# Optimization experiments

Hardware: AMD Instinct MI355X
Metric: run time of the kernel (lower is better)

The kernel has to match this reference:

```python
import jax, jax.numpy as jnp
import numpy as np

SPATIAL_SHAPES = np.array([[128, 128], [64, 64], [32, 32], [16, 16]], dtype=np.int32)  # (H, W) per level
D_MODEL = 256
D_FFN = 1024
N_LEVELS = 4
N_HEADS = 8
N_POINTS = 4
HEAD_DIM = D_MODEL // N_HEADS
B = 2
LEN = int((SPATIAL_SHAPES[:, 0] * SPATIAL_SHAPES[:, 1]).sum())  # 21760


def layer_norm(x, g, b, eps=1e-5):
    mu = x.mean(-1, keepdims=True)
    var = ((x - mu) ** 2).mean(-1, keepdims=True)
    return (x - mu) / jnp.sqrt(var + eps) * g + b


def ms_deform_attn_core(value, sampling_locations, attention_weights):
    # value: [B, Len, M, D]; locations: [B, Lq, M, L, P, 2] in [0,1]; weights: [B, Lq, M, L, P]
    B_, _, M, D = value.shape
    Lq = sampling_locations.shape[1]
    P = sampling_locations.shape[4]
    out = jnp.zeros((B_, M, Lq, D), value.dtype)
    start = 0
    for lvl, (H, W) in enumerate(SPATIAL_SHAPES.tolist()):
        v = value[:, start:start + H * W].transpose(0, 2, 1, 3)  # [B, M, H*W, D]
        start += H * W
        loc = sampling_locations[:, :, :, lvl].transpose(0, 2, 1, 3, 4)  # [B, M, Lq, P, 2]
        # grid_sample semantics: align_corners=False, padding_mode='zeros'
        x = loc[..., 0] * W - 0.5
        y = loc[..., 1] * H - 0.5
        x0 = jnp.floor(x)
        y0 = jnp.floor(y)
        wx = (x - x0)[..., None]
        wy = (y - y0)[..., None]

        def gather(xi, yi):
            valid = ((xi >= 0) & (xi < W) & (yi >= 0) & (yi < H)).astype(value.dtype)
            idx = (jnp.clip(yi, 0, H - 1) * W + jnp.clip(xi, 0, W - 1)).astype(jnp.int32)
            idx = idx.reshape(B_, M, Lq * P)
            g = jnp.take_along_axis(v, idx[..., None], axis=2).reshape(B_, M, Lq, P, D)
            return g * valid[..., None]

        v00 = gather(x0, y0)
        v01 = gather(x0 + 1, y0)
        v10 = gather(x0, y0 + 1)
        v11 = gather(x0 + 1, y0 + 1)
        samp = (v00 * (1 - wx) + v01 * wx) * (1 - wy) + (v10 * (1 - wx) + v11 * wx) * wy
        w_l = attention_weights[:, :, :, lvl].transpose(0, 2, 1, 3)  # [B, M, Lq, P]
        out = out + (samp * w_l[..., None]).sum(axis=3)
    return out.transpose(0, 2, 1, 3).reshape(B_, Lq, M * D)


def setup_inputs() -> dict:
    key = jax.random.key(0)
    ks = jax.random.split(key, 16)
    f32 = jnp.float32

    def lin(k, fan_in, fan_out, scale=None):
        s = scale if scale is not None else 1.0 / np.sqrt(fan_in)
        return jax.random.normal(k, (fan_in, fan_out), f32) * s

    starts = np.concatenate([[0], np.cumsum(SPATIAL_SHAPES[:, 0] * SPATIAL_SHAPES[:, 1])[:-1]]).astype(np.int32)
    inp = {
        "src": jax.random.normal(ks[0], (B, LEN, D_MODEL), f32),
        "pos": jax.random.normal(ks[1], (B, LEN, D_MODEL), f32),
        "reference_points": jax.random.uniform(ks[2], (B, LEN, N_LEVELS, 2), f32),
        "spatial_shapes": jnp.asarray(SPATIAL_SHAPES),
        "level_start_index": jnp.asarray(starts),
        "norm1_g": jnp.ones((D_MODEL,), f32), "norm1_b": jnp.zeros((D_MODEL,), f32),
        "norm2_g": jnp.ones((D_MODEL,), f32), "norm2_b": jnp.zeros((D_MODEL,), f32),
        "W_value": lin(ks[3], D_MODEL, D_MODEL), "b_value": jnp.zeros((D_MODEL,), f32),
        "W_off": lin(ks[4], D_MODEL, N_HEADS * N_LEVELS * N_POINTS * 2, scale=0.01),
        "b_off": jax.random.normal(ks[5], (N_HEADS * N_LEVELS * N_POINTS * 2,), f32) * 0.01,
        "W_attn": lin(ks[6], D_MODEL, N_HEADS * N_LEVELS * N_POINTS),
        "b_attn": jnp.zeros((N_HEADS * N_LEVELS * N_POINTS,), f32),
        "W_out": lin(ks[7], D_MODEL, D_MODEL), "b_out": jnp.zeros((D_MODEL,), f32),
        "W_ffn1": lin(ks[8], D_MODEL, D_FFN), "b_ffn1": jnp.zeros((D_FFN,), f32),
        "W_ffn2": lin(ks[9], D_FFN, D_MODEL), "b_ffn2": jnp.zeros((D_MODEL,), f32),
    }
    return inp


def reference(src, pos, reference_points, spatial_shapes, level_start_index,
              norm1_g, norm1_b, norm2_g, norm2_b,
              W_value, b_value, W_off, b_off, W_attn, b_attn, W_out, b_out,
              W_ffn1, b_ffn1, W_ffn2, b_ffn2):
    B_, Lq, C = src.shape
    # pre-norm deformable self-attention; NOTE: value path uses un-normed src (faithful to source)
    q = layer_norm(src, norm1_g, norm1_b) + pos
    value = (src @ W_value + b_value).reshape(B_, Lq, N_HEADS, HEAD_DIM)
    offsets = (q @ W_off + b_off).reshape(B_, Lq, N_HEADS, N_LEVELS, N_POINTS, 2)
    attn = jax.nn.softmax((q @ W_attn + b_attn).reshape(B_, Lq, N_HEADS, N_LEVELS * N_POINTS), axis=-1)
    attn = attn.reshape(B_, Lq, N_HEADS, N_LEVELS, N_POINTS)
    offset_normalizer = spatial_shapes[..., ::-1].astype(src.dtype)  # (W, H) per level
    loc = reference_points[:, :, None, :, None, :] + offsets / offset_normalizer[None, None, None, :, None, :]
    attn_out = ms_deform_attn_core(value, loc, attn) @ W_out + b_out
    src = src + attn_out
    h = layer_norm(src, norm2_g, norm2_b)
    h = jax.nn.gelu(h @ W_ffn1 + b_ffn1, approximate=False) @ W_ffn2 + b_ffn2
    return src + h
```

## Files before the change

kernel.cpp:

```cpp
#include <hip/hip_runtime.h>
#include <hip/hip_bf16.h>
#include <math.h>

#define LEN_TOT 21760
#define BATCH 2
#define MROWS (BATCH * LEN_TOT)
#define DMODEL 256
#define DFFN 1024

typedef unsigned short ushort_t;
typedef __attribute__((ext_vector_type(8))) short short8;
typedef __attribute__((ext_vector_type(4))) short short4v;
typedef __attribute__((ext_vector_type(4))) float floatx4;
typedef __attribute__((address_space(3))) ushort_t lds_us;
typedef __attribute__((address_space(1))) const ushort_t glb_us;

__device__ __forceinline__ ushort_t f2b(float f) {
    unsigned u = __float_as_uint(f);
    unsigned r = (u + 0x7FFFu + ((u >> 16) & 1u)) >> 16;
    return (ushort_t)r;
}
__device__ __forceinline__ float b2f(ushort_t u) {
    return __uint_as_float(((unsigned)u) << 16);
}

__device__ __forceinline__ float gelu_f(float x) {
    float x3 = x * x * x;
    float t = fmaf(x3, 0.035677408136f, x * 0.7978845608028654f);
    float e = __expf(2.0f * t);
    float th = 1.0f - 2.0f / (e + 1.0f);
    return 0.5f * x * (1.0f + th);
}

__device__ __forceinline__ int xcd_swizzle(int b, int n) {
    int q8 = n >> 3, r8 = n & 7;
    int xcd = b & 7, idx = b >> 3;
    return (xcd < r8 ? xcd * (q8 + 1) : r8 * (q8 + 1) + (xcd - r8) * q8) + idx;
}

template<int CTRL>
__device__ __forceinline__ float dpp_f(float x) {
    return __int_as_float(__builtin_amdgcn_update_dpp(
        0, __float_as_int(x), CTRL, 0xF, 0xF, true));
}
__device__ __forceinline__ float swz16_f(float x) {
    return __int_as_float(__builtin_amdgcn_ds_swizzle(__float_as_int(x), 0x401F));
}

struct TP {
    const float* s[6];
    ushort_t*    d[6];
    int K[6];
    int N[6];
    int start[7];
};

__global__ __launch_bounds__(256) void transpose_convert(TP tp) {
    __shared__ float tile[32][33];
    int blk = blockIdx.x;
    int seg = 0;
    while (seg < 5 && blk >= tp.start[seg + 1]) seg++;
    int local = blk - tp.start[seg];
    int K = tp.K[seg], N = tp.N[seg];
    int tn = N >> 5;
    int k0 = (local / tn) << 5, n0 = (local % tn) << 5;
    int r = threadIdx.x >> 5, c = threadIdx.x & 31;
    const float* src = tp.s[seg];
    #pragma unroll
    for (int rr = r; rr < 32; rr += 8)
        tile[rr][c] = src[(size_t)(k0 + rr) * N + n0 + c];
    __syncthreads();
    ushort_t* dst = tp.d[seg];
    #pragma unroll
    for (int rr = r; rr < 32; rr += 8)
        dst[(size_t)(n0 + rr) * K + k0 + c] = f2b(tile[c][rr]);
}

__global__ __launch_bounds__(256) void ln_dual_kernel(
    const float* __restrict__ x, const float* __restrict__ g,
    const float* __restrict__ bb, const float* __restrict__ addv,
    ushort_t* __restrict__ y_bf, ushort_t* __restrict__ x_bf)
{
    int row  = blockIdx.x * 4 + (threadIdx.x >> 6);
    int lane = threadIdx.x & 63;
    size_t base = (size_t)row * DMODEL + lane * 4;
    float4 v = *(const float4*)(x + base);

    float s = v.x + v.y + v.z + v.w;
    #pragma unroll
    for (int o = 32; o; o >>= 1) s += __shfl_xor(s, o, 64);
    float mu = s * (1.0f / 256.0f);

    float d0 = v.x - mu, d1 = v.y - mu, d2 = v.z - mu, d3 = v.w - mu;
    float vs = d0*d0 + d1*d1 + d2*d2 + d3*d3;
    #pragma unroll
    for (int o = 32; o; o >>= 1) vs += __shfl_xor(vs, o, 64);
    float rstd = rsqrtf(vs * (1.0f / 256.0f) + 1e-5f);

    float4 gv = *(const float4*)(g  + lane * 4);
    float4 bv = *(const float4*)(bb + lane * 4);
    float o0 = d0 * rstd * gv.x + bv.x;
    float o1 = d1 * rstd * gv.y + bv.y;
    float o2 = d2 * rstd * gv.z + bv.z;
    float o3 = d3 * rstd * gv.w + bv.w;
    if (addv) {
        float4 av = *(const float4*)(addv + base);
        o0 += av.x; o1 += av.y; o2 += av.z; o3 += av.w;
    }
    ushort4 ob = {f2b(o0), f2b(o1), f2b(o2), f2b(o3)};
    *(ushort4*)(y_bf + base) = ob;
    if (x_bf) {
        ushort4 xb = {f2b(v.x), f2b(v.y), f2b(v.z), f2b(v.w)};
        *(ushort4*)(x_bf + base) = xb;
    }
}

template<int GELU_ACT, int HAS_RES, int OUT_BF16>
__global__ __launch_bounds__(256) void gemm_mfma(
    const ushort_t* __restrict__ A, const ushort_t* __restrict__ Bt,
    const float* __restrict__ bias, const float* __restrict__ bias2, int bsplit,
    const float* __restrict__ res,
    float* __restrict__ C, ushort_t* __restrict__ Cbf,
    int M, int N, int K, int NX)
{
    constexpr int BM = 128, BK = 32;
    __shared__ __align__(16) ushort_t As[2][BM * BK];
    __shared__ __align__(16) ushort_t Bs[2][BM * BK];

    const int tid  = threadIdx.x;
    const int wave = tid >> 6;
    const int lane = tid & 63;
    const int wm = (wave & 1) * 64;
    const int wn = (wave >> 1) * 64;
    const int ml = lane & 15;
    const int quad = lane >> 4;
    const int w = xcd_swizzle(blockIdx.x, gridDim.x);
    const int bx = w % NX, by = w / NX;
    const int m0 = by * BM, n0 = bx * BM;

    const int r0 = tid >> 2, s0 = tid & 3;
    const int r1 = (tid + 256) >> 2;

    floatx4 acc[4][4] = {};

    auto stage = [&](int bsel, int k0) {
        const ushort_t* gA0 = A  + (size_t)(m0 + r0) * K + k0 + s0 * 8;
        const ushort_t* gA1 = A  + (size_t)(m0 + r1) * K + k0 + s0 * 8;
        const ushort_t* gB0 = Bt + (size_t)(n0 + r0) * K + k0 + s0 * 8;
        const ushort_t* gB1 = Bt + (size_t)(n0 + r1) * K + k0 + s0 * 8;
        __builtin_amdgcn_global_load_lds((glb_us*)gA0, (lds_us*)(As[bsel] + tid * 8),         16, 0, 0);
        __builtin_amdgcn_global_load_lds((glb_us*)gA1, (lds_us*)(As[bsel] + (tid + 256) * 8), 16, 0, 0);
        __builtin_amdgcn_global_load_lds((glb_us*)gB0, (lds_us*)(Bs[bsel] + tid * 8),         16, 0, 0);
        __builtin_amdgcn_global_load_lds((glb_us*)gB1, (lds_us*)(Bs[bsel] + (tid + 256) * 8), 16, 0, 0);
    };

    const int nt = K / BK;
    stage(0, 0);
    __syncthreads();

    int cur = 0;
    for (int t = 0; t < nt; ++t) {
        if (t + 1 < nt) stage(cur ^ 1, (t + 1) * BK);

        short8 af[4], bfr[4];
        #pragma unroll
        for (int i = 0; i < 4; i++)
            af[i] = *(const short8*)(As[cur] + (wm + i * 16 + ml) * BK + quad * 8);
        #pragma unroll
        for (int j = 0; j < 4; j++)
            bfr[j] = *(const short8*)(Bs[cur] + (wn + j * 16 + ml) * BK + quad * 8);
        #pragma unroll
        for (int i = 0; i < 4; i++)
            #pragma unroll
            for (int j = 0; j < 4; j++)
                acc[i][j] = __builtin_amdgcn_mfma_f32_16x16x32_bf16(
                    af[i], bfr[j], acc[i][j], 0, 0, 0);
        __syncthreads();
        cur ^= 1;
    }

    if constexpr (OUT_BF16) {
        constexpr int EST = 76;
        ushort_t* wb = &As[0][0] + wave * (16 * EST + 8);
        const int lr  = lane >> 2;
        const int sg  = lane & 3;
        #pragma unroll
        for (int i = 0; i < 4; i++) {
            #pragma unroll
            for (int j = 0; j < 4; j++) {
                int col = n0 + wn + j * 16 + ml;
                float bc = (col < bsplit) ? bias[col] : bias2[col - bsplit];
                #pragma unroll
                for (int r = 0; r < 4; r++) {
                    float v = acc[i][j][r] + bc;
                    if (GELU_ACT) v = gelu_f(v);
                    if (HAS_RES)
                        v += res[(size_t)(m0 + wm + i * 16 + quad * 4 + r) * N
                                 + n0 + wn + j * 16 + ml];
                    wb[(quad * 4 + r) * EST + j * 16 + ml] = f2b(v);
                }
            }
            asm volatile("s_waitcnt lgkmcnt(0)" ::: "memory");
            #pragma unroll
            for (int h = 0; h < 2; h++) {
                int off = lr * EST + (sg + 4 * h) * 8;
                short4v lo = *(const short4v*)(wb + off);
                short4v hi = *(const short4v*)(wb + off + 4);
                short8 vv;
                vv[0] = lo[0]; vv[1] = lo[1]; vv[2] = lo[2]; vv[3] = lo[3];
                vv[4] = hi[0]; vv[5] = hi[1]; vv[6] = hi[2]; vv[7] = hi[3];
                *(short8*)(Cbf + (size_t)(m0 + wm + i * 16 + lr) * N
                                 + n0 + wn + (sg + 4 * h) * 8) = vv;
            }
        }
    } else {
        #pragma unroll
        for (int j = 0; j < 4; j++) {
            int col = n0 + wn + j * 16 + ml;
            float bc = (col < bsplit) ? bias[col] : bias2[col - bsplit];
            #pragma unroll
            for (int i = 0; i < 4; i++) {
                int row = m0 + wm + i * 16 + quad * 4;
                #pragma unroll
                for (int r = 0; r < 4; r++) {
                    float v = acc[i][j][r] + bc;
                    if (GELU_ACT) v = gelu_f(v);
                    if (HAS_RES) v += res[(size_t)(row + r) * N + col];
                    C[(size_t)(row + r) * N + col] = v;
                }
            }
        }
    }
}

__global__ __launch_bounds__(256) void msdeform_kernel(
    const ushort_t* __restrict__ value, const float* __restrict__ comb,
    const float* __restrict__ refp, ushort_t* __restrict__ out_bf)
{
    int blk = xcd_swizzle(blockIdx.x, gridDim.x);
    int gid = blk * 8 + (threadIdx.x >> 5);
    int l   = threadIdx.x & 31;
    int bq  = gid >> 3;
    int m   = gid & 7;
    int b   = (bq >= LEN_TOT) ? 1 : 0;

    int i = l & 15;
    float logit = comb[(size_t)bq * 384 + 256 + m * 16 + i];
    float mx = logit;
    mx = fmaxf(mx, dpp_f<0x128>(mx));
    mx = fmaxf(mx, dpp_f<0x124>(mx));
    mx = fmaxf(mx, dpp_f<0x122>(mx));
    mx = fmaxf(mx, dpp_f<0x121>(mx));
    float e = __expf(logit - mx);
    float se = e;
    se += dpp_f<0x128>(se);
    se += dpp_f<0x124>(se);
    se += dpp_f<0x122>(se);
    se += dpp_f<0x121>(se);
    float prob = e / se;

    const int ST_[4] = {0, 16384, 20480, 21504};
    const int sA = (l >> 2) & 7;
    const int cA = l & 3;
    const int dx = cA & 1, dy = cA >> 1;
    float probA = __shfl(prob, sA, 32);
    float probB = __shfl(prob, sA + 8, 32);

    int aA, aB; float hA, hB;
    #define CORNER(S, PROB, ADDR, WGT) { \
        int lvl = (S) >> 2; \
        int Wl = 128 >> lvl; float Wf = (float)Wl; \
        float2 off2 = ((const float2*)comb)[(size_t)bq * 192 + m * 16 + (S)]; \
        float2 ref2 = ((const float2*)refp)[(size_t)bq * 4 + lvl]; \
        float xs = fmaf(ref2.x, Wf, off2.x) - 0.5f; \
        float ys = fmaf(ref2.y, Wf, off2.y) - 0.5f; \
        float xf = floorf(xs), yf = floorf(ys); \
        int x0 = (int)xf, y0 = (int)yf; \
        float wx = xs - xf, wy = ys - yf; \
        int xc = x0 + dx, yc = y0 + dy; \
        bool v = (xc >= 0) & (xc < Wl) & (yc >= 0) & (yc < Wl); \
        int cx = min(max(xc, 0), Wl - 1); \
        int cy = min(max(yc, 0), Wl - 1); \
        ADDR = (b * LEN_TOT + ST_[lvl] + cy * Wl + cx) * 512 + m * 64; \
        float wxe = dx ? wx : 1.0f - wx; \
        float wye = dy ? wy : 1.0f - wy; \
        WGT = v ? (PROB) * wxe * wye : 0.0f; }
    CORNER(sA,     probA, aA, hA)
    CORNER(sA + 8, probB, aB, hB)
    #undef CORNER

    const int cl2 = l >> 2;
    const int dof = (l & 3) * 16;

    int p0 = __shfl(aA,      cl2, 32) + dof;
    int p1 = __shfl(aA,  8 + cl2, 32) + dof;
    int p2 = __shfl(aA, 16 + cl2, 32) + dof;
    int p3 = __shfl(aA, 24 + cl2, 32) + dof;
    int p4 = __shfl(aB,      cl2, 32) + dof;
    int p5 = __shfl(aB,  8 + cl2, 32) + dof;
    int p6 = __shfl(aB, 16 + cl2, 32) + dof;
    int p7 = __shfl(aB, 24 + cl2, 32) + dof;
    float h0 = __shfl(hA,      cl2, 32);
    float h1 = __shfl(hA,  8 + cl2, 32);
    float h2 = __shfl(hA, 16 + cl2, 32);
    float h3 = __shfl(hA, 24 + cl2, 32);
    float h4 = __shfl(hB,      cl2, 32);
    float h5 = __shfl(hB,  8 + cl2, 32);
    float h6 = __shfl(hB, 16 + cl2, 32);
    float h7 = __shfl(hB, 24 + cl2, 32);

    const char* vb = (const char*)value;
    uint4 v0 = *(const uint4*)(vb + p0);
    uint4 v1 = *(const uint4*)(vb + p1);
    uint4 v2 = *(const uint4*)(vb + p2);
    uint4 v3 = *(const uint4*)(vb + p3);
    uint4 v4 = *(const uint4*)(vb + p4);
    uint4 v5 = *(const uint4*)(vb + p5);
    uint4 v6 = *(const uint4*)(vb + p6);
    uint4 v7 = *(const uint4*)(vb + p7);

    float c0 = 0, c1 = 0, c2 = 0, c3 = 0, c4 = 0, c5 = 0, c6 = 0, c7 = 0;
    #define ACC8(V, H) \
        c0 = fmaf(H, __uint_as_float((V).x << 16),         c0); \
        c1 = fmaf(H, __uint_as_float((V).x & 0xffff0000u), c1); \
        c2 = fmaf(H, __uint_as_float((V).y << 16),         c2); \
        c3 = fmaf(H, __uint_as_float((V).y & 0xffff0000u), c3); \
        c4 = fmaf(H, __uint_as_float((V).z << 16),         c4); \
        c5 = fmaf(H, __uint_as_float((V).z & 0xffff0000u), c5); \
        c6 = fmaf(H, __uint_as_float((V).w << 16),         c6); \
        c7 = fmaf(H, __uint_as_float((V).w & 0xffff0000u), c7);
    ACC8(v0, h0) ACC8(v1, h1) ACC8(v2, h2) ACC8(v3, h3)
    ACC8(v4, h4) ACC8(v5, h5) ACC8(v6, h6) ACC8(v7, h7)
    #undef ACC8

    c0 += dpp_f<0x124>(c0); c1 += dpp_f<0x124>(c1);
    c2 += dpp_f<0x124>(c2); c3 += dpp_f<0x124>(c3);
    c4 += dpp_f<0x124>(c4); c5 += dpp_f<0x124>(c5);
    c6 += dpp_f<0x124>(c6); c7 += dpp_f<0x124>(c7);
    c0 += dpp_f<0x128>(c0); c1 += dpp_f<0x128>(c1);
    c2 += dpp_f<0x128>(c2); c3 += dpp_f<0x128>(c3);
    c4 += dpp_f<0x128>(c4); c5 += dpp_f<0x128>(c5);
    c6 += dpp_f<0x128>(c6); c7 += dpp_f<0x128>(c7);
    c0 += swz16_f(c0); c1 += swz16_f(c1);
    c2 += swz16_f(c2); c3 += swz16_f(c3);
    c4 += swz16_f(c4); c5 += swz16_f(c5);
    c6 += swz16_f(c6); c7 += swz16_f(c7);

    if (l < 4) {
        short8 ov;
        ov[0] = (short)f2b(c0); ov[1] = (short)f2b(c1);
        ov[2] = (short)f2b(c2); ov[3] = (short)f2b(c3);
        ov[4] = (short)f2b(c4); ov[5] = (short)f2b(c5);
        ov[6] = (short)f2b(c6); ov[7] = (short)f2b(c7);
        *(short8*)(out_bf + (size_t)gid * 32 + l * 8) = ov;
    }
}

extern "C" void kernel_launch(void* const* d_in, const int* in_sizes, int n_in,
                              void* d_out, int out_size, void* d_ws, size_t ws_size,
                              hipStream_t stream)
{
    const float* src  = (const float*)d_in[0];
    const float* pos  = (const float*)d_in[1];
    const float* refp = (const float*)d_in[2];
    const float* n1g = (const float*)d_in[5];
    const float* n1b = (const float*)d_in[6];
    const float* n2g = (const float*)d_in[7];
    const float* n2b = (const float*)d_in[8];
    const float* Wv  = (const float*)d_in[9];
    const float* bv  = (const float*)d_in[10];
    const float* Wof = (const float*)d_in[11];
    const float* bof = (const float*)d_in[12];
    const float* Wat = (const float*)d_in[13];
    const float* bat = (const float*)d_in[14];
    const float* Wo  = (const float*)d_in[15];
    const float* bo  = (const float*)d_in[16];
    const float* Wf1 = (const float*)d_in[17];
    const float* bf1 = (const float*)d_in[18];
    const float* Wf2 = (const float*)d_in[19];
    const float* bf2 = (const float*)d_in[20];
    float* out = (float*)d_out;

    char* ws = (char*)d_ws;
    const int M = MROWS;
    const size_t SZ_BF = (size_t)M * 256 * 2;
    const size_t SZ_F  = (size_t)M * 256 * 4;
    const int BIG = 1 << 30;

    ushort_t* q_bf    = (ushort_t*)(ws);
    ushort_t* value_b = (ushort_t*)(ws + SZ_BF);
    ushort_t* src_bf  = (ushort_t*)(ws + SZ_BF + SZ_F);
    float*    comb    = (float*)   (ws + 2 * SZ_BF + SZ_F);
    ushort_t* h0_bf   = q_bf;
    ushort_t* sampled = src_bf;
    float*    src2    = (float*)   (ws + SZ_BF);
    ushort_t* h1_bf   = src_bf;
    char* wtp = ws + 2 * SZ_BF + 2 * SZ_F + (size_t)M * 128 * 4;
    ushort_t* WvT  = (ushort_t*)(wtp);
    ushort_t* WofT = WvT  + 256 * 256;
    ushort_t* WatT = WofT + 256 * 256;
    ushort_t* WoT  = WatT + 256 * 128;
    ushort_t* Wf1T = WoT  + 256 * 256;
    ushort_t* Wf2T = Wf1T + 256 * 1024;

    TP tp;
    tp.s[0] = Wv;  tp.d[0] = WvT;  tp.K[0] = 256;  tp.N[0] = 256;
    tp.s[1] = Wof; tp.d[1] = WofT; tp.K[1] = 256;  tp.N[1] = 256;
    tp.s[2] = Wat; tp.d[2] = WatT; tp.K[2] = 256;  tp.N[2] = 128;
    tp.s[3] = Wo;  tp.d[3] = WoT;  tp.K[3] = 256;  tp.N[3] = 256;
    tp.s[4] = Wf1; tp.d[4] = Wf1T; tp.K[4] = 256;  tp.N[4] = 1024;
    tp.s[5] = Wf2; tp.d[5] = Wf2T; tp.K[5] = 1024; tp.N[5] = 256;
    tp.start[0] = 0;   tp.start[1] = 64;  tp.start[2] = 128;
    tp.start[3] = 160; tp.start[4] = 224; tp.start[5] = 480; tp.start[6] = 736;
    transpose_convert<<<736, 256, 0, stream>>>(tp);

    ln_dual_kernel<<<M / 4, 256, 0, stream>>>(src, n1g, n1b, pos, q_bf, src_bf);
    gemm_mfma<0, 0, 1><<<2 * (M / 128), 256, 0, stream>>>(
        src_bf, WvT, bv, bv, BIG, nullptr, nullptr, value_b, M, 256, 256, 2);
    gemm_mfma<0, 0, 0><<<3 * (M / 128), 256, 0, stream>>>(
        q_bf, WofT, bof, bat, 256, nullptr, comb, nullptr, M, 384, 256, 3);
    msdeform_kernel<<<M, 256, 0, stream>>>(value_b, comb, refp, sampled);
    gemm_mfma<0, 1, 0><<<2 * (M / 128), 256, 0, stream>>>(
        sampled, WoT, bo, bo, BIG, src, src2, nullptr, M, 256, 256, 2);
    ln_dual_kernel<<<M / 4, 256, 0, stream>>>(src2, n2g, n2b, nullptr, h0_bf, nullptr);
    gemm_mfma<1, 0, 1><<<8 * (M / 128), 256, 0, stream>>>(
        h0_bf, Wf1T, bf1, bf1, BIG, nullptr, nullptr, h1_bf, M, 1024, 256, 8);
    gemm_mfma<0, 1, 0><<<2 * (M / 128), 256, 0, stream>>>(
        h1_bf, Wf2T, bf2, bf2, BIG, src2, out, nullptr, M, 256, 1024, 2);
}
```

Baseline: 434.7 us.

## Fuse FFN up-projection, GELU and down-projection into one kernel

```diff
diff --git a/kernel.cpp b/kernel.cpp
--- a/kernel.cpp
+++ b/kernel.cpp
@@ -228,6 +228,125 @@
                     if (HAS_RES) v += res[(size_t)(row + r) * N + col];
                     C[(size_t)(row + r) * N + col] = v;
                 }
+            }
+        }
+    }
+}
+
+__global__ __launch_bounds__(256) void ffn_fused(
+    const ushort_t* __restrict__ h0, const ushort_t* __restrict__ Wf1T,
+    const float* __restrict__ b1, const ushort_t* __restrict__ Wf2T,
+    const float* __restrict__ b2, const float* __restrict__ res,
+    float* __restrict__ out, int M)
+{
+    constexpr int BM = 128, BK = 32, TST = 136;
+    __shared__ __align__(16) ushort_t As[2][BM * BK];
+    __shared__ __align__(16) ushort_t Bs[2][BM * BK];
+    __shared__ __align__(16) ushort_t Ts[BM * TST];
+
+    const int tid  = threadIdx.x;
+    const int wave = tid >> 6;
+    const int lane = tid & 63;
+    const int wm = (wave & 1) * 64;
+    const int wn = (wave >> 1) * 64;
+    const int ml = lane & 15;
+    const int quad = lane >> 4;
+    const int w = xcd_swizzle(blockIdx.x, gridDim.x);
+    const int bx = w % 2, by = w / 2;
+    const int m0 = by * BM, n0 = bx * BM;
+
+    const int r0 = tid >> 2, s0 = tid & 3;
+    const int r1 = (tid + 256) >> 2;
+
+    floatx4 accO[4][4] = {};
+
+    for (int c = 0; c < 8; ++c) {
+        floatx4 accT[4][4] = {};
+        auto stageA = [&](int bsel, int k0) {
+            const ushort_t* gA0 = h0 + (size_t)(m0 + r0) * 256 + k0 + s0 * 8;
+            const ushort_t* gA1 = h0 + (size_t)(m0 + r1) * 256 + k0 + s0 * 8;
+            const ushort_t* gB0 = Wf1T + (size_t)(c * 128 + r0) * 256 + k0 + s0 * 8;
+            const ushort_t* gB1 = Wf1T + (size_t)(c * 128 + r1) * 256 + k0 + s0 * 8;
+            __builtin_amdgcn_global_load_lds((glb_us*)gA0, (lds_us*)(As[bsel] + tid * 8),         16, 0, 0);
+            __builtin_amdgcn_global_load_lds((glb_us*)gA1, (lds_us*)(As[bsel] + (tid + 256) * 8), 16, 0, 0);
+            __builtin_amdgcn_global_load_lds((glb_us*)gB0, (lds_us*)(Bs[bsel] + tid * 8),         16, 0, 0);
+            __builtin_amdgcn_global_load_lds((glb_us*)gB1, (lds_us*)(Bs[bsel] + (tid + 256) * 8), 16, 0, 0);
+        };
+        stageA(0, 0);
+        __syncthreads();
+        int cur = 0;
+        #pragma unroll
+        for (int t = 0; t < 8; ++t) {
+            if (t + 1 < 8) stageA(cur ^ 1, (t + 1) * BK);
+            short8 af[4], bfr[4];
+            #pragma unroll
+            for (int i = 0; i < 4; i++)
+                af[i] = *(const short8*)(As[cur] + (wm + i * 16 + ml) * BK + quad * 8);
+            #pragma unroll
+            for (int j = 0; j < 4; j++)
+                bfr[j] = *(const short8*)(Bs[cur] + (wn + j * 16 + ml) * BK + quad * 8);
+            #pragma unroll
+            for (int i = 0; i < 4; i++)
+                #pragma unroll
+                for (int j = 0; j < 4; j++)
+                    accT[i][j] = __builtin_amdgcn_mfma_f32_16x16x32_bf16(
+                        af[i], bfr[j], accT[i][j], 0, 0, 0);
+            __syncthreads();
+            cur ^= 1;
+        }
+        #pragma unroll
+        for (int i = 0; i < 4; i++)
+            #pragma unroll
+            for (int j = 0; j < 4; j++) {
+                int col = wn + j * 16 + ml;
+                float bc = b1[c * 128 + col];
+                #pragma unroll
+                for (int r = 0; r < 4; r++) {
+                    float v = gelu_f(accT[i][j][r] + bc);
+                    Ts[(wm + i * 16 + quad * 4 + r) * TST + col] = f2b(v);
+                }
+            }
+        auto stageB = [&](int bsel, int kk0) {
+            const ushort_t* gB0 = Wf2T + (size_t)(n0 + r0) * 1024 + c * 128 + kk0 + s0 * 8;
+            const ushort_t* gB1 = Wf2T + (size_t)(n0 + r1) * 1024 + c * 128 + kk0 + s0 * 8;
+            __builtin_amdgcn_global_load_lds((glb_us*)gB0, (lds_us*)(Bs[bsel] + tid * 8),         16, 0, 0);
+            __builtin_amdgcn_global_load_lds((glb_us*)gB1, (lds_us*)(Bs[bsel] + (tid + 256) * 8), 16, 0, 0);
+        };
+        stageB(0, 0);
+        __syncthreads();
+        cur = 0;
+        #pragma unroll
+        for (int tt = 0; tt < 4; ++tt) {
+            if (tt + 1 < 4) stageB(cur ^ 1, (tt + 1) * BK);
+            short8 af[4], bfr[4];
+            #pragma unroll
+            for (int i = 0; i < 4; i++)
+                af[i] = *(const short8*)(Ts + (wm + i * 16 + ml) * TST + tt * BK + quad * 8);
+            #pragma unroll
+            for (int j = 0; j < 4; j++)
+                bfr[j] = *(const short8*)(Bs[cur] + (wn + j * 16 + ml) * BK + quad * 8);
+            #pragma unroll
+            for (int i = 0; i < 4; i++)
+                #pragma unroll
+                for (int j = 0; j < 4; j++)
+                    accO[i][j] = __builtin_amdgcn_mfma_f32_16x16x32_bf16(
+                        af[i], bfr[j], accO[i][j], 0, 0, 0);
+            __syncthreads();
+            cur ^= 1;
+        }
+    }
+
+    #pragma unroll
+    for (int j = 0; j < 4; j++) {
+        int col = n0 + wn + j * 16 + ml;
+        float bc = b2[col];
+        #pragma unroll
+        for (int i = 0; i < 4; i++) {
+            int row = m0 + wm + i * 16 + quad * 4;
+            #pragma unroll
+            for (int r = 0; r < 4; r++) {
+                out[(size_t)(row + r) * 256 + col] =
+                    accO[i][j][r] + bc + res[(size_t)(row + r) * 256 + col];
             }
         }
     }
@@ -394,7 +513,6 @@
     ushort_t* h0_bf   = q_bf;
     ushort_t* sampled = src_bf;
     float*    src2    = (float*)   (ws + SZ_BF);
-    ushort_t* h1_bf   = src_bf;
     char* wtp = ws + 2 * SZ_BF + 2 * SZ_F + (size_t)M * 128 * 4;
     ushort_t* WvT  = (ushort_t*)(wtp);
     ushort_t* WofT = WvT  + 256 * 256;
@@ -423,8 +541,6 @@
     gemm_mfma<0, 1, 0><<<2 * (M / 128), 256, 0, stream>>>(
         sampled, WoT, bo, bo, BIG, src, src2, nullptr, M, 256, 256, 2);
     ln_dual_kernel<<<M / 4, 256, 0, stream>>>(src2, n2g, n2b, nullptr, h0_bf, nullptr);
-    gemm_mfma<1, 0, 1><<<8 * (M / 128), 256, 0, stream>>>(
-        h0_bf, Wf1T, bf1, bf1, BIG, nullptr, nullptr, h1_bf, M, 1024, 256, 8);
-    gemm_mfma<0, 1, 0><<<2 * (M / 128), 256, 0, stream>>>(
-        h1_bf, Wf2T, bf2, bf2, BIG, src2, out, nullptr, M, 256, 1024, 2);
-}
+    ffn_fused<<<2 * (M / 128), 256, 0, stream>>>(
+        h0_bf, Wf1T, bf1, Wf2T, bf2, src2, out, M);
+}
```

Measured after the change: 500.2 us. 1.15x slower.
